# Kernel optimization log

Hardware: AMD Instinct MI355X
Metric: run time of the kernel (lower is better)

## Reference

```python
import jax, jax.numpy as jnp
import numpy as np

EPS = 1e-5

def _hdc_branch(emb, w, b, dil, ln_g, ln_b):
    # emb: [N, L, E]; w: [K, E, F] ('WIO'); same-length dilated conv
    y = jax.lax.conv_general_dilated(
        emb, w, window_strides=(1,), padding=[(dil, dil)],
        rhs_dilation=(dil,), dimension_numbers=('NWC', 'WIO', 'NWC')) + b
    m = y.mean(-1, keepdims=True)
    v = ((y - m) ** 2).mean(-1, keepdims=True)
    y = (y - m) / jnp.sqrt(v + EPS) * ln_g + ln_b
    return jax.nn.relu(y)  # [N, L, F]

def _news_encoder(titles, embedding, w1, b1, w2, b2, w3, b3, ln_g, ln_b,
                  q_levels, q_words):
    B, n, L = titles.shape
    E = embedding.shape[-1]
    emb = embedding[titles].reshape(B * n, L, E)  # dropout = identity (eval)
    d = jnp.stack([
        _hdc_branch(emb, w1, b1, 1, ln_g, ln_b),
        _hdc_branch(emb, w2, b2, 2, ln_g, ln_b),
        _hdc_branch(emb, w3, b3, 3, ln_g, ln_b),
    ], axis=2)  # [Bn, L, 3, F]
    F = d.shape[-1]
    d = d.reshape(B, n, L, 3, F)
    scale = jnp.sqrt(jnp.asarray(E, d.dtype))  # original divides by sqrt(embedding_dim)
    # level-wise attention pooling (1-row query over 3 levels)
    wl = jax.nn.softmax(jnp.einsum('f,bnlkf->bnlk', q_levels[0], d) / scale, axis=-1)
    attn = jnp.einsum('bnlk,bnlkf->bnlf', wl, d)  # [B, n, L, F]
    # word-wise attention pooling (1-row query over L words)
    ww = jax.nn.softmax(jnp.einsum('f,bnlf->bnl', q_words[0], attn) / scale, axis=-1)
    reprs = jnp.einsum('bnl,bnlf->bnf', ww, attn)  # [B, n, F]
    return reprs

def setup_inputs() -> dict:
    key = jax.random.key(0)
    ks = jax.random.split(key, 12)
    V, E, F, H = 50000, 300, 150, 50
    return {
        'candidate_title': jax.random.randint(ks[0], (64, 5, 30), 0, V),
        'clicked_title': jax.random.randint(ks[1], (64, H, 30), 0, V),
        'embedding': jax.random.normal(ks[2], (V, E), jnp.float32),
        'w1': jax.random.normal(ks[3], (3, E, F), jnp.float32) * 0.05,
        'b1': jax.random.normal(ks[4], (F,), jnp.float32) * 0.05,
        'w2': jax.random.normal(ks[5], (3, E, F), jnp.float32) * 0.05,
        'b2': jax.random.normal(ks[6], (F,), jnp.float32) * 0.05,
        'w3': jax.random.normal(ks[7], (3, E, F), jnp.float32) * 0.05,
        'b3': jax.random.normal(ks[8], (F,), jnp.float32) * 0.05,
        'ln_g': jnp.ones((F,), jnp.float32),
        'ln_b': jnp.zeros((F,), jnp.float32),
        'q_levels': jax.random.normal(ks[9], (1, F), jnp.float32),
        'q_words': jax.random.normal(ks[10], (1, F), jnp.float32),
        'ltr_w': jax.random.normal(ks[11], (1, H), jnp.float32) * 0.1,
        'ltr_b': jnp.zeros((1,), jnp.float32),
    }

def reference(candidate_title, clicked_title, embedding, w1, b1, w2, b2, w3, b3,
              ln_g, ln_b, q_levels, q_words, ltr_w, ltr_b):
    cdd = _news_encoder(candidate_title, embedding, w1, b1, w2, b2, w3, b3,
                        ln_g, ln_b, q_levels, q_words)  # [B, cdd, F]
    his = _news_encoder(clicked_title, embedding, w1, b1, w2, b2, w3, b3,
                        ln_g, ln_b, q_levels, q_words)  # [B, his, F]
    scores = jnp.einsum('bcf,bhf->bch', cdd, his)        # [B, cdd, his]
    logits = jnp.einsum('bch,oh->bco', scores, ltr_w)[..., 0] + ltr_b[0]  # [B, cdd]
    return jax.nn.log_softmax(logits, axis=1)  # cdd_size > 1 branch
```

## Files before the change

kernel.cpp:

```cpp
#include <hip/hip_runtime.h>

typedef unsigned short u16;
typedef unsigned int   u32;
typedef __bf16 bf16x8 __attribute__((ext_vector_type(8)));
typedef float  f32x4  __attribute__((ext_vector_type(4)));
typedef _Float16 h2 __attribute__((ext_vector_type(2)));

#define M_ROWS 50000
#define M_PAD  50176
#define M_TILES 196
#define N_REAL 1368
#define N_PAD  1536
#define N_TILES64 22
#define K_DIM  300
#define K_PAD  320
#define KT     10
#define TROW   1408
#define SEG    152
#define YCOL   152

#define GLDS(gp, lp) __builtin_amdgcn_global_load_lds( \
    (const __attribute__((address_space(1))) void*)(gp), \
    (__attribute__((address_space(3))) void*)(lp), 16, 0, 0)

static __device__ __forceinline__ u16 f2bf(float x){
  union { float f; u32 u; } a; a.f = x;
  u32 r = a.u + 0x7fffu + ((a.u >> 16) & 1u);
  return (u16)(r >> 16);
}
static __device__ __forceinline__ u16 f2h(float x){
  _Float16 h = (_Float16)x;
  u16 r; __builtin_memcpy(&r, &h, 2); return r;
}
static __device__ __forceinline__ float h2f(u16 v){
  _Float16 h; __builtin_memcpy(&h, &v, 2); return (float)h;
}

static __device__ __forceinline__ float wsum63(float x){
  asm volatile(
    "s_nop 1\n\t"
    "v_add_f32 %0, %0, %0 row_shr:1 bound_ctrl:0\n\t"
    "s_nop 1\n\t"
    "v_add_f32 %0, %0, %0 row_shr:2 bound_ctrl:0\n\t"
    "s_nop 1\n\t"
    "v_add_f32 %0, %0, %0 row_shr:4 bound_ctrl:0\n\t"
    "s_nop 1\n\t"
    "v_add_f32 %0, %0, %0 row_shr:8 bound_ctrl:0\n\t"
    "s_nop 1\n\t"
    "v_add_f32 %0, %0, %0 row_bcast:15 row_mask:0xa\n\t"
    "s_nop 1\n\t"
    "v_add_f32 %0, %0, %0 row_bcast:31 row_mask:0xc\n\t"
    "s_nop 1"
    : "+v"(x));
  return x;
}
static __device__ __forceinline__ float wmax63(float x){
  asm volatile(
    "s_nop 1\n\t"
    "v_max_f32 %0, %0, %0 row_shr:1\n\t"
    "s_nop 1\n\t"
    "v_max_f32 %0, %0, %0 row_shr:2\n\t"
    "s_nop 1\n\t"
    "v_max_f32 %0, %0, %0 row_shr:4\n\t"
    "s_nop 1\n\t"
    "v_max_f32 %0, %0, %0 row_shr:8\n\t"
    "s_nop 1\n\t"
    "v_max_f32 %0, %0, %0 row_bcast:15 row_mask:0xa\n\t"
    "s_nop 1\n\t"
    "v_max_f32 %0, %0, %0 row_bcast:31 row_mask:0xc\n\t"
    "s_nop 1"
    : "+v"(x));
  return x;
}
static __device__ __forceinline__ float rdl63(float x){
  union { float f; int i; } a; a.f = x;
  union { int i; float f; } r; r.i = __builtin_amdgcn_readlane(a.i, 63);
  return r.f;
}

__global__ __launch_bounds__(256) void build_A(const float* __restrict__ emb, u16* __restrict__ A){
  __shared__ __align__(16) u16 st[8192];
  const int blk = blockIdx.x;
  const int tile = blk / KT, kt = blk % KT;
  const int tid = threadIdx.x;
  const int m0 = tile * 256, k0 = kt * 32;
  #pragma unroll
  for (int u = 0; u < 8; ++u){
    int i = tid + u * 256;
    int r = i >> 3, c = i & 7;
    int m = m0 + r, k = k0 + c * 4;
    float4 v = (float4){0.f, 0.f, 0.f, 0.f};
    if (m < M_ROWS && k < K_DIM)
      v = *(const float4*)(emb + (size_t)m * K_DIM + k);
    int dst = (r >> 4) * 512 + (c >> 1) * 128 + (r & 15) * 8 + (c & 1) * 4;
    union { u32 d[2]; u16 s[4]; } w;
    w.s[0] = f2bf(v.x); w.s[1] = f2bf(v.y); w.s[2] = f2bf(v.z); w.s[3] = f2bf(v.w);
    *(uint2*)(st + dst) = *(const uint2*)w.d;
  }
  __syncthreads();
  u16* out = A + ((size_t)tile * KT + kt) * 8192;
  #pragma unroll
  for (int q = 0; q < 4; ++q){
    int o = tid * 8 + q * 2048;
    *(uint4*)(out + o) = *(const uint4*)(st + o);
  }
}

__global__ void build_B(const float* __restrict__ w1, const float* __restrict__ w2,
                        const float* __restrict__ w3, u16* __restrict__ B){
  int t = blockIdx.x * 256 + threadIdx.x;
  if (t >= N_PAD * K_PAD) return;
  int n = t / K_PAD, k = t % K_PAD;
  float x = 0.f;
  if (n < N_REAL && k < K_DIM){
    int br = n / 456, rem = n % 456, tap = rem / 152, f = rem % 152;
    if (f < 150){
      const float* w = (br == 0) ? w1 : ((br == 1) ? w2 : w3);
      x = w[(tap * K_DIM + k) * 150 + f];
    }
  }
  int tn = n >> 7, nl = n & 127, nb = nl >> 4, col = nl & 15;
  int kt = k >> 5, kl = k & 31, kg = kl >> 3, k8 = kl & 7;
  B[((size_t)tn * KT + kt) * 4096 + nb * 512 + kg * 128 + col * 8 + k8] = f2bf(x);
}

__global__ __launch_bounds__(256, 6) void gemm_k(const u16* __restrict__ A, const u16* __restrict__ B,
                                                 u16* __restrict__ T){
  __shared__ __align__(16) u16 lds[12288];
  const int flat = blockIdx.x;
  const int xcd = flat & 7, ord = flat >> 3;
  const int wg = xcd * 1078 + ord;
  const int tn = wg % 22, tM = wg / 22;
  const int t256 = tM >> 1, hM = tM & 1;
  const int tn128 = tn >> 1, h64 = tn & 1;
  const int tid = threadIdx.x, wave = tid >> 6, lane = tid & 63;
  const int wm = wave >> 1, wn = wave & 1;
  f32x4 acc[4][2];
  #pragma unroll
  for (int i = 0; i < 4; ++i)
    #pragma unroll
    for (int j = 0; j < 2; ++j) acc[i][j] = (f32x4){0.f, 0.f, 0.f, 0.f};
  const u16* Ab = A + ((size_t)t256 * KT) * 8192 + hM * 4096;
  const u16* Bb = B + ((size_t)tn128 * KT) * 4096 + h64 * 2048;
  GLDS(Ab + tid * 8,        lds + tid * 8);
  GLDS(Ab + 2048 + tid * 8, lds + 2048 + tid * 8);
  GLDS(Bb + tid * 8,        lds + 4096 + tid * 8);
  #pragma unroll
  for (int s = 0; s < 10; ++s){
    const int b = s & 1;
    u16* cur = lds + b * 6144;
    if (s < 9){
      u16* nxt = lds + (b ^ 1) * 6144;
      GLDS(Ab + (s + 1) * 8192 + tid * 8,        nxt + tid * 8);
      GLDS(Ab + (s + 1) * 8192 + 2048 + tid * 8, nxt + 2048 + tid * 8);
      GLDS(Bb + (s + 1) * 4096 + tid * 8,        nxt + 4096 + tid * 8);
      asm volatile("s_waitcnt vmcnt(3)" ::: "memory");
    } else {
      asm volatile("s_waitcnt vmcnt(0)" ::: "memory");
    }
    __builtin_amdgcn_sched_barrier(0);
    __builtin_amdgcn_s_barrier();
    const bf16x8* A8 = (const bf16x8*)cur;
    const bf16x8* B8 = (const bf16x8*)(cur + 4096);
    bf16x8 av[4], bv[2];
    #pragma unroll
    for (int i = 0; i < 4; ++i) av[i] = A8[(wm * 4 + i) * 64 + lane];
    #pragma unroll
    for (int j = 0; j < 2; ++j) bv[j] = B8[(wn * 2 + j) * 64 + lane];
    #pragma unroll
    for (int i = 0; i < 4; ++i)
      #pragma unroll
      for (int j = 0; j < 2; ++j)
        acc[i][j] = __builtin_amdgcn_mfma_f32_16x16x32_bf16(av[i], bv[j], acc[i][j], 0, 0, 0);
    __builtin_amdgcn_s_barrier();
  }
  const int r0 = (lane >> 4) * 4, c0 = lane & 15;
  const int row = tid >> 2, q = tid & 3;
  #pragma unroll
  for (int h = 0; h < 2; ++h){
    __syncthreads();
    if (wm == h){
      #pragma unroll
      for (int i = 0; i < 4; ++i){
        #pragma unroll
        for (int j = 0; j < 2; ++j){
          int col = wn * 32 + j * 16 + c0;
          #pragma unroll
          for (int r = 0; r < 4; ++r)
            lds[(i * 16 + r0 + r) * 72 + col] = f2h(acc[i][j][r]);
        }
      }
    }
    __syncthreads();
    int m = tM * 128 + h * 64 + row;
    if (m < M_ROWS){
      const u16* src = lds + row * 72 + q * 16;
      u16* dst = T + (size_t)m * TROW + tn * 64 + q * 16;
      *(uint4*)(dst)     = *(const uint4*)(src);
      *(uint4*)(dst + 8) = *(const uint4*)(src + 8);
    }
  }
}

__global__ __launch_bounds__(512, 4) void encode_k(
    const int* __restrict__ cand, const int* __restrict__ clk,
    const u16* __restrict__ T,
    const float* __restrict__ b1, const float* __restrict__ b2, const float* __restrict__ b3,
    const float* __restrict__ lng, const float* __restrict__ lnb,
    const float* __restrict__ ql, const float* __restrict__ qw,
    float* __restrict__ rc, float* __restrict__ rh){
  __shared__ __align__(16) u16 ybuf[90][YCOL];
  __shared__ float tl[32];
  __shared__ float pbuf[8][YCOL];
  __shared__ u32 wordoff[32];
  const int t = blockIdx.x;
  const int tid = threadIdx.x, wave = tid >> 6, lane = tid & 63;
  const int* wp; float* outp;
  if (t < 320){ wp = cand + t * 30;                outp = rc + t * 150; }
  else        { wp = clk + (size_t)(t - 320) * 30; outp = rh + (size_t)(t - 320) * 150; }
  if (tid < 30) wordoff[tid] = (u32)wp[tid] * (u32)TROW;
  __syncthreads();
  const float invs = 0.057735026918962576f;
  const int f0 = lane, f1 = lane + 64, f2 = lane + 128;
  const bool has2 = (f2 < 150);

  uint4 rv[12]; bool vm[12]; int pA[4], fgA[4]; bool ivA[4];
  #pragma unroll
  for (int it = 0; it < 4; ++it){
    const int item = tid + it * 512;
    const bool iv = item < 1710;
    const int p = item / 19, fg = item - p * 19;
    pA[it] = p; fgA[it] = fg; ivA[it] = iv;
    const int l = p / 3, br = p - l * 3, dil = br + 1;
    #pragma unroll
    for (int tap = 0; tap < 3; ++tap){
      const int ls = l + (tap - 1) * dil;
      const int lsc = ls < 0 ? 0 : (ls > 29 ? 29 : ls);
      vm[it * 3 + tap] = iv && (ls >= 0) && (ls < 30);
      rv[it * 3 + tap] = *(const uint4*)(T + wordoff[lsc] + br * 456 + tap * SEG + fg * 8);
    }
  }
  #pragma unroll
  for (int it = 0; it < 4; ++it){
    if (ivA[it]){
      union { uint4 q; h2 h[4]; } s, va, vb, vc;
      const uint4 z4 = (uint4){0u, 0u, 0u, 0u};
      va.q = vm[it * 3]     ? rv[it * 3]     : z4;
      vb.q = vm[it * 3 + 1] ? rv[it * 3 + 1] : z4;
      vc.q = vm[it * 3 + 2] ? rv[it * 3 + 2] : z4;
      #pragma unroll
      for (int i = 0; i < 4; ++i) s.h[i] = va.h[i] + vb.h[i] + vc.h[i];
      *(uint4*)&ybuf[pA[it]][fgA[it] * 8] = s.q;
    }
  }

  float qlv0 = ql[f0], qlv1 = ql[f1], qlv2 = has2 ? ql[f2] : 0.f;
  float qwv0 = qw[f0], qwv1 = qw[f1], qwv2 = has2 ? qw[f2] : 0.f;
  float lg0 = lng[f0], lg1 = lng[f1], lg2 = has2 ? lng[f2] : 0.f;
  float lb0 = lnb[f0], lb1 = lnb[f1], lb2 = has2 ? lnb[f2] : 0.f;
  float bs[3][3];
  {
    const float* bl[3] = {b1, b2, b3};
    #pragma unroll
    for (int br = 0; br < 3; ++br){
      bs[br][0] = bl[br][f0]; bs[br][1] = bl[br][f1]; bs[br][2] = has2 ? bl[br][f2] : 0.f;
    }
  }
  __syncthreads();

  float at0[4], at1[4], at2[4];
  #pragma unroll
  for (int q = 0; q < 4; ++q){
    const int l = wave + q * 8;
    at0[q] = 0.f; at1[q] = 0.f; at2[q] = 0.f;
    if (l < 30){
      float dr[3][3]; float lvl[3];
      #pragma unroll
      for (int br = 0; br < 3; ++br){
        int p = l * 3 + br;
        float y0 = h2f(ybuf[p][f0]) + bs[br][0];
        float y1 = h2f(ybuf[p][f1]) + bs[br][1];
        float y2 = has2 ? (h2f(ybuf[p][f2]) + bs[br][2]) : 0.f;
        float s  = y0 + y1 + y2;
        float ss = y0 * y0 + y1 * y1 + y2 * y2;
        float st = wsum63(s), sst = wsum63(ss);
        float mean = rdl63(st) * (1.f / 150.f);
        float var  = rdl63(sst) * (1.f / 150.f) - mean * mean;
        float rstd = rsqrtf(var + 1e-5f);
        float d0 = fmaxf((y0 - mean) * rstd * lg0 + lb0, 0.f);
        float d1 = fmaxf((y1 - mean) * rstd * lg1 + lb1, 0.f);
        float d2 = has2 ? fmaxf((y2 - mean) * rstd * lg2 + lb2, 0.f) : 0.f;
        dr[br][0] = d0; dr[br][1] = d1; dr[br][2] = d2;
        float dot = qlv0 * d0 + qlv1 * d1 + qlv2 * d2;
        lvl[br] = rdl63(wsum63(dot)) * invs;
      }
      float mx = fmaxf(lvl[0], fmaxf(lvl[1], lvl[2]));
      float e0 = __expf(lvl[0] - mx), e1 = __expf(lvl[1] - mx), e2 = __expf(lvl[2] - mx);
      float inv = 1.f / (e0 + e1 + e2);
      float w0 = e0 * inv, w1v = e1 * inv, w2v = e2 * inv;
      float a0 = w0 * dr[0][0] + w1v * dr[1][0] + w2v * dr[2][0];
      float a1 = w0 * dr[0][1] + w1v * dr[1][1] + w2v * dr[2][1];
      float a2 = w0 * dr[0][2] + w1v * dr[1][2] + w2v * dr[2][2];
      float dot = qwv0 * a0 + qwv1 * a1 + qwv2 * a2;
      float tw = wsum63(dot);
      if (lane == 63) tl[l] = tw * invs;
      at0[q] = a0; at1[q] = a1; at2[q] = a2;
    }
  }
  __syncthreads();

  if (wave == 0){
    float v = (lane < 30) ? tl[lane] : -1e30f;
    float mx = rdl63(wmax63(v));
    float e = (lane < 30) ? __expf(v - mx) : 0.f;
    float den = rdl63(wsum63(e));
    if (lane < 30) tl[lane] = e / den;
  }
  __syncthreads();

  float p0 = 0.f, p1 = 0.f, p2 = 0.f;
  #pragma unroll
  for (int q = 0; q < 4; ++q){
    const int l = wave + q * 8;
    if (l < 30){
      float wwv = tl[l];
      p0 += wwv * at0[q]; p1 += wwv * at1[q]; p2 += wwv * at2[q];
    }
  }
  pbuf[wave][lane] = p0;
  pbuf[wave][lane + 64] = p1;
  if (has2) pbuf[wave][lane + 128] = p2;
  __syncthreads();
  if (tid < 150){
    float acc = 0.f;
    #pragma unroll
    for (int w = 0; w < 8; ++w) acc += pbuf[w][tid];
    outp[tid] = acc;
  }
}

__global__ __launch_bounds__(256) void final_k(const float* __restrict__ rc, const float* __restrict__ rh,
                                               const float* __restrict__ lw, const float* __restrict__ lb,
                                               float* __restrict__ out){
  __shared__ float Cl[750];
  __shared__ float Hl[7500];
  __shared__ float sc[5][52];
  __shared__ float lg[5];
  const int b = blockIdx.x, tid = threadIdx.x;
  const float* C = rc + b * 750;
  const float* H = rh + (size_t)b * 7500;
  for (int i = tid; i < 750; i += 256) Cl[i] = C[i];
  for (int i = tid; i < 7500; i += 256) Hl[i] = H[i];
  __syncthreads();
  if (tid < 250){
    int c = tid / 50, h = tid % 50;
    float s = 0.f;
    #pragma unroll 10
    for (int k = 0; k < 150; ++k) s += Cl[c * 150 + k] * Hl[h * 150 + k];
    sc[c][h] = s;
  }
  __syncthreads();
  if (tid < 5){
    float s = lb[0];
    for (int h = 0; h < 50; ++h) s += sc[tid][h] * lw[h];
    lg[tid] = s;
  }
  __syncthreads();
  if (tid < 5){
    float mx = fmaxf(fmaxf(fmaxf(lg[0], lg[1]), fmaxf(lg[2], lg[3])), lg[4]);
    float den = 0.f;
    for (int c = 0; c < 5; ++c) den += expf(lg[c] - mx);
    out[b * 5 + tid] = lg[tid] - mx - logf(den);
  }
}

extern "C" void kernel_launch(void* const* d_in, const int* in_sizes, int n_in,
                              void* d_out, int out_size, void* d_ws, size_t ws_size,
                              hipStream_t stream){
  const int*   cand = (const int*)d_in[0];
  const int*   clk  = (const int*)d_in[1];
  const float* emb  = (const float*)d_in[2];
  const float* w1   = (const float*)d_in[3];
  const float* b1   = (const float*)d_in[4];
  const float* w2   = (const float*)d_in[5];
  const float* b2   = (const float*)d_in[6];
  const float* w3   = (const float*)d_in[7];
  const float* b3   = (const float*)d_in[8];
  const float* lng  = (const float*)d_in[9];
  const float* lnb  = (const float*)d_in[10];
  const float* ql   = (const float*)d_in[11];
  const float* qw   = (const float*)d_in[12];
  const float* lw   = (const float*)d_in[13];
  const float* lb   = (const float*)d_in[14];
  float* out = (float*)d_out;

  char* ws = (char*)d_ws;
  const size_t szA = (size_t)M_TILES * KT * 16384;
  const size_t szB = (size_t)12 * KT * 8192;
  const size_t szT = (size_t)M_ROWS * TROW * 2;
  u16*   A  = (u16*)ws;
  u16*   B  = (u16*)(ws + szA);
  u16*   T  = (u16*)(ws + szA + szB);
  float* rc = (float*)(ws + szA + szB + szT);
  float* rh = rc + 320 * 150;

  build_A<<<M_TILES * KT, 256, 0, stream>>>(emb, A);
  build_B<<<(N_PAD * K_PAD + 255) / 256, 256, 0, stream>>>(w1, w2, w3, B);
  gemm_k<<<dim3(392 * N_TILES64), 256, 0, stream>>>(A, B, T);
  encode_k<<<3520, 512, 0, stream>>>(cand, clk, T, b1, b2, b3, lng, lnb, ql, qw, rc, rh);
  final_k<<<64, 256, 0, stream>>>(rc, rh, lw, lb, out);
}
```

Before: 254.9 us.

## Merge A/B build kernels, single-buffer GEMM with larger K-steps, nontemporal stores

Folds build_A and build_B into one launch so a kernel launch and its tail go away. The GEMM main loop drops its double-buffered prefetch for a single buffer holding two K-slices per stage, with full barriers around each load. This halves the stage count but stops overlapping loads with MFMA work, and the occupancy hint drops from 6 to 5. Output stores to T become nontemporal so they do not pollute the cache.

```diff
diff --git a/kernel.cpp b/kernel.cpp
--- a/kernel.cpp
+++ b/kernel.cpp
@@ -5,6 +5,7 @@
 typedef __bf16 bf16x8 __attribute__((ext_vector_type(8)));
 typedef float  f32x4  __attribute__((ext_vector_type(4)));
 typedef _Float16 h2 __attribute__((ext_vector_type(2)));
+typedef u32 u32x4 __attribute__((ext_vector_type(4)));
 
 #define M_ROWS 50000
 #define M_PAD  50176
@@ -18,6 +19,8 @@
 #define TROW   1408
 #define SEG    152
 #define YCOL   152
+#define NBLKA  1960
+#define NBLKB  1920
 
 #define GLDS(gp, lp) __builtin_amdgcn_global_load_lds( \
     (const __attribute__((address_space(1))) void*)(gp), \
@@ -78,53 +81,56 @@
   return r.f;
 }
 
-__global__ __launch_bounds__(256) void build_A(const float* __restrict__ emb, u16* __restrict__ A){
+__global__ __launch_bounds__(256) void build_AB(const float* __restrict__ emb,
+                                                const float* __restrict__ w1,
+                                                const float* __restrict__ w2,
+                                                const float* __restrict__ w3,
+                                                u16* __restrict__ A, u16* __restrict__ B){
   __shared__ __align__(16) u16 st[8192];
   const int blk = blockIdx.x;
-  const int tile = blk / KT, kt = blk % KT;
   const int tid = threadIdx.x;
-  const int m0 = tile * 256, k0 = kt * 32;
-  #pragma unroll
-  for (int u = 0; u < 8; ++u){
-    int i = tid + u * 256;
-    int r = i >> 3, c = i & 7;
-    int m = m0 + r, k = k0 + c * 4;
-    float4 v = (float4){0.f, 0.f, 0.f, 0.f};
-    if (m < M_ROWS && k < K_DIM)
-      v = *(const float4*)(emb + (size_t)m * K_DIM + k);
-    int dst = (r >> 4) * 512 + (c >> 1) * 128 + (r & 15) * 8 + (c & 1) * 4;
-    union { u32 d[2]; u16 s[4]; } w;
-    w.s[0] = f2bf(v.x); w.s[1] = f2bf(v.y); w.s[2] = f2bf(v.z); w.s[3] = f2bf(v.w);
-    *(uint2*)(st + dst) = *(const uint2*)w.d;
-  }
-  __syncthreads();
-  u16* out = A + ((size_t)tile * KT + kt) * 8192;
-  #pragma unroll
-  for (int q = 0; q < 4; ++q){
-    int o = tid * 8 + q * 2048;
-    *(uint4*)(out + o) = *(const uint4*)(st + o);
-  }
-}
-
-__global__ void build_B(const float* __restrict__ w1, const float* __restrict__ w2,
-                        const float* __restrict__ w3, u16* __restrict__ B){
-  int t = blockIdx.x * 256 + threadIdx.x;
-  if (t >= N_PAD * K_PAD) return;
-  int n = t / K_PAD, k = t % K_PAD;
-  float x = 0.f;
-  if (n < N_REAL && k < K_DIM){
-    int br = n / 456, rem = n % 456, tap = rem / 152, f = rem % 152;
-    if (f < 150){
-      const float* w = (br == 0) ? w1 : ((br == 1) ? w2 : w3);
-      x = w[(tap * K_DIM + k) * 150 + f];
-    }
-  }
-  int tn = n >> 7, nl = n & 127, nb = nl >> 4, col = nl & 15;
-  int kt = k >> 5, kl = k & 31, kg = kl >> 3, k8 = kl & 7;
-  B[((size_t)tn * KT + kt) * 4096 + nb * 512 + kg * 128 + col * 8 + k8] = f2bf(x);
-}
-
-__global__ __launch_bounds__(256, 6) void gemm_k(const u16* __restrict__ A, const u16* __restrict__ B,
+  if (blk < NBLKA){
+    const int tile = blk / KT, kt = blk % KT;
+    const int m0 = tile * 256, k0 = kt * 32;
+    #pragma unroll
+    for (int u = 0; u < 8; ++u){
+      int i = tid + u * 256;
+      int r = i >> 3, c = i & 7;
+      int m = m0 + r, k = k0 + c * 4;
+      float4 v = (float4){0.f, 0.f, 0.f, 0.f};
+      if (m < M_ROWS && k < K_DIM)
+        v = *(const float4*)(emb + (size_t)m * K_DIM + k);
+      int dst = (r >> 4) * 512 + (c >> 1) * 128 + (r & 15) * 8 + (c & 1) * 4;
+      union { u32 d[2]; u16 s[4]; } w;
+      w.s[0] = f2bf(v.x); w.s[1] = f2bf(v.y); w.s[2] = f2bf(v.z); w.s[3] = f2bf(v.w);
+      *(uint2*)(st + dst) = *(const uint2*)w.d;
+    }
+    __syncthreads();
+    u16* out = A + ((size_t)tile * KT + kt) * 8192;
+    #pragma unroll
+    for (int q = 0; q < 4; ++q){
+      int o = tid * 8 + q * 2048;
+      *(uint4*)(out + o) = *(const uint4*)(st + o);
+    }
+  } else {
+    int t = (blk - NBLKA) * 256 + tid;
+    if (t >= N_PAD * K_PAD) return;
+    int n = t / K_PAD, k = t % K_PAD;
+    float x = 0.f;
+    if (n < N_REAL && k < K_DIM){
+      int br = n / 456, rem = n % 456, tap = rem / 152, f = rem % 152;
+      if (f < 150){
+        const float* w = (br == 0) ? w1 : ((br == 1) ? w2 : w3);
+        x = w[(tap * K_DIM + k) * 150 + f];
+      }
+    }
+    int tn = n >> 7, nl = n & 127, nb = nl >> 4, col = nl & 15;
+    int kt = k >> 5, kl = k & 31, kg = kl >> 3, k8 = kl & 7;
+    B[((size_t)tn * KT + kt) * 4096 + nb * 512 + kg * 128 + col * 8 + k8] = f2bf(x);
+  }
+}
+
+__global__ __launch_bounds__(256, 5) void gemm_k(const u16* __restrict__ A, const u16* __restrict__ B,
                                                  u16* __restrict__ T){
   __shared__ __align__(16) u16 lds[12288];
   const int flat = blockIdx.x;
@@ -142,37 +148,31 @@
     for (int j = 0; j < 2; ++j) acc[i][j] = (f32x4){0.f, 0.f, 0.f, 0.f};
   const u16* Ab = A + ((size_t)t256 * KT) * 8192 + hM * 4096;
   const u16* Bb = B + ((size_t)tn128 * KT) * 4096 + h64 * 2048;
-  GLDS(Ab + tid * 8,        lds + tid * 8);
-  GLDS(Ab + 2048 + tid * 8, lds + 2048 + tid * 8);
-  GLDS(Bb + tid * 8,        lds + 4096 + tid * 8);
-  #pragma unroll
-  for (int s = 0; s < 10; ++s){
-    const int b = s & 1;
-    u16* cur = lds + b * 6144;
-    if (s < 9){
-      u16* nxt = lds + (b ^ 1) * 6144;
-      GLDS(Ab + (s + 1) * 8192 + tid * 8,        nxt + tid * 8);
-      GLDS(Ab + (s + 1) * 8192 + 2048 + tid * 8, nxt + 2048 + tid * 8);
-      GLDS(Bb + (s + 1) * 4096 + tid * 8,        nxt + 4096 + tid * 8);
-      asm volatile("s_waitcnt vmcnt(3)" ::: "memory");
-    } else {
-      asm volatile("s_waitcnt vmcnt(0)" ::: "memory");
-    }
-    __builtin_amdgcn_sched_barrier(0);
-    __builtin_amdgcn_s_barrier();
-    const bf16x8* A8 = (const bf16x8*)cur;
-    const bf16x8* B8 = (const bf16x8*)(cur + 4096);
-    bf16x8 av[4], bv[2];
-    #pragma unroll
-    for (int i = 0; i < 4; ++i) av[i] = A8[(wm * 4 + i) * 64 + lane];
-    #pragma unroll
-    for (int j = 0; j < 2; ++j) bv[j] = B8[(wn * 2 + j) * 64 + lane];
-    #pragma unroll
-    for (int i = 0; i < 4; ++i)
-      #pragma unroll
-      for (int j = 0; j < 2; ++j)
-        acc[i][j] = __builtin_amdgcn_mfma_f32_16x16x32_bf16(av[i], bv[j], acc[i][j], 0, 0, 0);
-    __builtin_amdgcn_s_barrier();
+  #pragma unroll
+  for (int s = 0; s < 5; ++s){
+    __syncthreads();
+    GLDS(Ab + s * 16384 + tid * 8,               lds + tid * 8);
+    GLDS(Ab + s * 16384 + 2048 + tid * 8,        lds + 2048 + tid * 8);
+    GLDS(Ab + s * 16384 + 8192 + tid * 8,        lds + 4096 + tid * 8);
+    GLDS(Ab + s * 16384 + 8192 + 2048 + tid * 8, lds + 6144 + tid * 8);
+    GLDS(Bb + s * 8192 + tid * 8,                lds + 8192 + tid * 8);
+    GLDS(Bb + s * 8192 + 4096 + tid * 8,         lds + 10240 + tid * 8);
+    __syncthreads();
+    #pragma unroll
+    for (int kk = 0; kk < 2; ++kk){
+      const bf16x8* A8 = (const bf16x8*)(lds + kk * 4096);
+      const bf16x8* B8 = (const bf16x8*)(lds + 8192 + kk * 2048);
+      bf16x8 av[4], bv[2];
+      #pragma unroll
+      for (int i = 0; i < 4; ++i) av[i] = A8[(wm * 4 + i) * 64 + lane];
+      #pragma unroll
+      for (int j = 0; j < 2; ++j) bv[j] = B8[(wn * 2 + j) * 64 + lane];
+      #pragma unroll
+      for (int i = 0; i < 4; ++i)
+        #pragma unroll
+        for (int j = 0; j < 2; ++j)
+          acc[i][j] = __builtin_amdgcn_mfma_f32_16x16x32_bf16(av[i], bv[j], acc[i][j], 0, 0, 0);
+    }
   }
   const int r0 = (lane >> 4) * 4, c0 = lane & 15;
   const int row = tid >> 2, q = tid & 3;
@@ -196,8 +196,8 @@
     if (m < M_ROWS){
       const u16* src = lds + row * 72 + q * 16;
       u16* dst = T + (size_t)m * TROW + tn * 64 + q * 16;
-      *(uint4*)(dst)     = *(const uint4*)(src);
-      *(uint4*)(dst + 8) = *(const uint4*)(src + 8);
+      __builtin_nontemporal_store(*(const u32x4*)(src),     (u32x4*)(dst));
+      __builtin_nontemporal_store(*(const u32x4*)(src + 8), (u32x4*)(dst + 8));
     }
   }
 }
@@ -404,8 +404,7 @@
   float* rc = (float*)(ws + szA + szB + szT);
   float* rh = rc + 320 * 150;
 
-  build_A<<<M_TILES * KT, 256, 0, stream>>>(emb, A);
-  build_B<<<(N_PAD * K_PAD + 255) / 256, 256, 0, stream>>>(w1, w2, w3, B);
+  build_AB<<<NBLKA + NBLKB, 256, 0, stream>>>(emb, w1, w2, w3, A, B);
   gemm_k<<<dim3(392 * N_TILES64), 256, 0, stream>>>(A, B, T);
   encode_k<<<3520, 512, 0, stream>>>(cand, clk, T, b1, b2, b3, lng, lnb, ql, qw, rc, rh);
   final_k<<<64, 256, 0, stream>>>(rc, rh, lw, lb, out);
```

Result: slower. 265.7 us (+4.2%).
